# Kernel optimization log

Hardware: AMD Instinct MI355X
Metric: run time of the kernel (lower is better)

Reference implementation:

```python
import jax, jax.numpy as jnp
import numpy as np

EMBED_DIM = 1024
NUM_HEADS = 16
HEAD_DIM = EMBED_DIM // NUM_HEADS
B, S = 2, 2048
BIG = 1e9  # clamp / nan_to_num saturation value from the torch module


def setup_inputs() -> dict:
    key = jax.random.key(0)
    k1, k2, k3, k4, k5 = jax.random.split(key, 5)
    sc = 1.0 / np.sqrt(EMBED_DIM)
    x = jax.random.normal(k1, (B, S, EMBED_DIM), dtype=jnp.float32)
    qkv_w = jax.random.normal(k2, (3 * EMBED_DIM, EMBED_DIM), dtype=jnp.float32) * sc
    qkv_b = jax.random.normal(k3, (3 * EMBED_DIM,), dtype=jnp.float32) * 0.01
    out_w = jax.random.normal(k4, (EMBED_DIM, EMBED_DIM), dtype=jnp.float32) * sc
    out_b = jax.random.normal(k5, (EMBED_DIM,), dtype=jnp.float32) * 0.01
    # causal mask, broadcastable to [B, H, S, S]; 0 => masked
    mask = jnp.tril(jnp.ones((S, S), dtype=jnp.int32))[None, None, :, :]
    return {"x": x, "mask": mask, "qkv_w": qkv_w, "qkv_b": qkv_b,
            "out_w": out_w, "out_b": out_b}


def reference(x, mask, qkv_w, qkv_b, out_w, out_b):
    b, s, e = x.shape
    # fused QKV projection (torch Linear: x @ W.T + b)
    qkv = x @ qkv_w.T + qkv_b                      # [B, S, 3E]
    q, k, v = jnp.split(qkv, 3, axis=-1)
    def heads(t):
        return t.reshape(b, s, NUM_HEADS, HEAD_DIM).transpose(0, 2, 1, 3)  # [B,H,S,D]
    q, k, v = heads(q), heads(k), heads(v)
    scores = jnp.einsum('bhqd,bhkd->bhqk', q, k) / np.sqrt(HEAD_DIM)
    scores = jnp.clip(scores, -BIG, BIG)
    # masked_fill(mask==0, -inf) then nan_to_num(neginf=-1e9) => masked -> -1e9
    scores = jnp.where(mask == 0, -jnp.inf, scores)
    scores = jnp.nan_to_num(scores, nan=0.0, posinf=BIG, neginf=-BIG)
    scores = scores - jnp.max(scores, axis=-1, keepdims=True)
    attn = jax.nn.softmax(scores, axis=-1) + 1e-9
    out = jnp.einsum('bhqk,bhkd->bhqd', attn, v)   # [B,H,S,D]
    out = out.transpose(0, 2, 1, 3).reshape(b, s, e)
    return out @ out_w.T + out_b
```

## Files before the change

### kernel.cpp

```cpp
#include <hip/hip_runtime.h>
#include <stdint.h>

#define B_ 2
#define H_ 16
#define S_ 2048
#define D_ 64
#define E_ 1024
#define M_ 4096
#define N3_ 3072

typedef __attribute__((ext_vector_type(8))) short bf16x8;
typedef __attribute__((ext_vector_type(4))) float f32x4;
typedef __attribute__((ext_vector_type(16))) float f32x16;
typedef __attribute__((ext_vector_type(4))) unsigned short us4;
typedef __attribute__((ext_vector_type(4))) int i32x4;

__device__ __forceinline__ unsigned short f2b(float f) {
  union { float f; unsigned int u; } v; v.f = f;
  unsigned int r = v.u + 0x7FFFu + ((v.u >> 16) & 1u);
  return (unsigned short)(r >> 16);
}

__device__ __forceinline__ void gll16(const void* g, void* l) {
  __builtin_amdgcn_global_load_lds((const __attribute__((address_space(1))) uint32_t*)g,
                                   (__attribute__((address_space(3))) uint32_t*)l, 16, 0, 0);
}

__global__ __launch_bounds__(256) void f32_to_bf16_k(const float* __restrict__ in,
                                                     unsigned short* __restrict__ out, int n) {
  int i = (blockIdx.x * blockDim.x + threadIdx.x) * 4;
  if (i + 3 < n) {
    float4 v = *(const float4*)(in + i);
    us4 o; o.x = f2b(v.x); o.y = f2b(v.y); o.z = f2b(v.z); o.w = f2b(v.w);
    *(us4*)(out + i) = o;
  }
}

template<int MODE>
__global__ __launch_bounds__(512)
void gemm_bt_k(const unsigned short* __restrict__ A,
               const unsigned short* __restrict__ Bw,
               const float* __restrict__ bias,
               float* __restrict__ outf,
               unsigned short* __restrict__ qo,
               unsigned short* __restrict__ ko,
               unsigned short* __restrict__ vto,
               const int K) {
  __shared__ unsigned short As[2][128 * 32];
  __shared__ unsigned short Bs[2][128 * 32];
  const int tid = threadIdx.x;
  const int wid = tid >> 6, lane = tid & 63;
  const int l4 = lane & 15, lh = lane >> 4;
  const int gx = gridDim.x;
  int id = blockIdx.y * gx + blockIdx.x;
  const int cpx = (gx * gridDim.y) >> 3;
  id = (id & 7) * cpx + (id >> 3);
  const int bm = (id / gx) << 7, bn = (id % gx) << 7;
  const int mq = wid >> 2, nq = wid & 3;
  const int wm = mq << 6, wn = nq << 5;
  f32x4 acc[4][2] = {};
  const int srow = lane >> 2;
  const int scolb = ((lane & 3) ^ (((lane >> 3) & 1) << 1)) << 4;
  auto STAGE = [&](int bb, int kt) {
    const int r = (wid << 4) + srow;
    gll16((const char*)A + ((size_t)(bm + r) * K + kt) * 2 + scolb, &As[bb][wid << 9]);
    gll16((const char*)Bw + ((size_t)(bn + r) * K + kt) * 2 + scolb, &Bs[bb][wid << 9]);
  };
  STAGE(0, 0);
  __syncthreads();
  const int ro = (l4 << 5) + ((lh ^ (((l4 >> 1) & 1) << 1)) << 3);
  for (int kt = 0; kt < K; kt += 32) {
    const int bb = (kt >> 5) & 1;
    if (kt + 32 < K) STAGE(bb ^ 1, kt + 32);
    bf16x8 af[4], bfr[2];
#pragma unroll
    for (int g = 0; g < 4; ++g)
      af[g] = *(const bf16x8*)&As[bb][(((mq << 2) + g) << 9) + ro];
#pragma unroll
    for (int h = 0; h < 2; ++h)
      bfr[h] = *(const bf16x8*)&Bs[bb][(((nq << 1) + h) << 9) + ro];
#pragma unroll
    for (int mg = 0; mg < 4; ++mg)
#pragma unroll
      for (int ng = 0; ng < 2; ++ng)
        acc[mg][ng] = __builtin_amdgcn_mfma_f32_16x16x32_bf16(af[mg], bfr[ng], acc[mg][ng], 0, 0, 0);
    __syncthreads();
  }
#pragma unroll
  for (int mg = 0; mg < 4; ++mg) {
#pragma unroll
    for (int ng = 0; ng < 2; ++ng) {
      const int n = bn + wn + (ng << 4) + l4;
      const float bv = bias[n];
      const int m0 = bm + wm + (mg << 4) + (lh << 2);
      if (MODE == 1) {
#pragma unroll
        for (int i = 0; i < 4; ++i)
          outf[(size_t)(m0 + i) * E_ + n] = acc[mg][ng][i] + bv;
      } else {
        const int region = n >> 10;
        const int nn = n & 1023;
        const int h = nn >> 6, d = nn & 63;
        const int b = m0 >> 11, s0 = m0 & 2047;
        const int bh = (b << 4) + h;
        if (region == 2) {
          us4 pk;
#pragma unroll
          for (int i = 0; i < 4; ++i) pk[i] = f2b(acc[mg][ng][i] + bv);
          *(us4*)&vto[((size_t)bh * D_ + d) * S_ + s0] = pk;
        } else {
          unsigned short* dst = (region == 0) ? qo : ko;
          const float sc = (region == 0) ? 0.125f : 1.0f;
#pragma unroll
          for (int i = 0; i < 4; ++i)
            dst[((size_t)bh * S_ + s0 + i) * D_ + d] = f2b((acc[mg][ng][i] + bv) * sc);
        }
      }
    }
  }
}

__global__ __launch_bounds__(256)
void attn_k(const unsigned short* __restrict__ Q,
            const unsigned short* __restrict__ Kt,
            const unsigned short* __restrict__ Vt,
            unsigned short* __restrict__ O) {
  __shared__ __align__(16) char smem[32768];
  const int tid = threadIdx.x;
  const int wid = tid >> 6, lane = tid & 63;
  const int l31 = lane & 31, hi = lane >> 5, hi4 = hi << 2;
  const int bid = blockIdx.x;
  const int xcd = bid & 7, ii = bid >> 3;
  const int bh = (xcd << 2) + (ii & 3);
  const int j = ii >> 2;
  const int qb = (j < 8) ? (15 - j) : (j - 8);
  const int q0w = (qb << 7) + (wid << 5);
  const int nt = (qb + 1) << 1;
  const int ntaw = ((q0w + 31) >> 6) + 1;

  const char* Qb = (const char*)Q + (size_t)bh * (S_ * D_ * 2);
  const char* Kb = (const char*)Kt + (size_t)bh * (S_ * D_ * 2);
  const char* Vb = (const char*)Vt + (size_t)bh * (D_ * S_ * 2);

  bf16x8 qf[4];
#pragma unroll
  for (int st = 0; st < 4; ++st)
    qf[st] = *(const bf16x8*)(Qb + (size_t)(q0w + l31) * 128 + (st << 5) + (hi << 4));

  const int r1 = (wid << 4) + (lane >> 3), r2 = r1 + 8;
  const int cc = lane & 7;
  const int ko1 = (r1 << 7) + ((cc ^ (r1 & 7)) << 4);
  const int ko2 = (r2 << 7) + ((cc ^ (r2 & 7)) << 4);
  const int vo1 = (r1 << 12) + ((cc ^ (r1 & 7)) << 4);
  const int vo2 = (r2 << 12) + ((cc ^ (r2 & 7)) << 4);

  f32x16 oacc[2] = {};
  float m_i = -3.0e38f, l_i = 0.0f;
  const int qg = q0w + l31;
  const int swl = l31 & 7;

  {
    char* kd = smem + (wid << 11);
    char* vd = smem + 16384 + (wid << 11);
    gll16(Kb + ko1, kd); gll16(Kb + ko2, kd + 1024);
    gll16(Vb + vo1, vd); gll16(Vb + vo2, vd + 1024);
  }
  __syncthreads();

  for (int t = 0; t < nt; ++t) {
    const int cur = t & 1;
    if (t + 1 < nt) {
      const int nb = cur ^ 1;
      char* kd = smem + (nb << 13) + (wid << 11);
      char* vd = smem + 16384 + (nb << 13) + (wid << 11);
      gll16(Kb + (size_t)(t + 1) * 8192 + ko1, kd);
      gll16(Kb + (size_t)(t + 1) * 8192 + ko2, kd + 1024);
      gll16(Vb + (size_t)(t + 1) * 128 + vo1, vd);
      gll16(Vb + (size_t)(t + 1) * 128 + vo2, vd + 1024);
    }
    if (t < ntaw) {
      const char* Kc = smem + (cur << 13);
      const char* Vc = smem + 16384 + (cur << 13);
      f32x16 sacc[2] = {};
#pragma unroll
      for (int tt = 0; tt < 2; ++tt)
#pragma unroll
        for (int st = 0; st < 4; ++st) {
          bf16x8 kf = *(const bf16x8*)(Kc + (tt << 12) + (l31 << 7) + ((((st << 1) + hi) ^ swl) << 4));
          sacc[tt] = __builtin_amdgcn_mfma_f32_32x32x16_bf16(kf, qf[st], sacc[tt], 0, 0, 0);
        }
      if (t == ntaw - 1) {
        const int kv0 = t << 6;
#pragma unroll
        for (int tt = 0; tt < 2; ++tt)
#pragma unroll
          for (int r = 0; r < 16; ++r) {
            const int kg = kv0 + (tt << 5) + (r & 3) + ((r >> 2) << 3) + hi4;
            if (kg > qg) sacc[tt][r] = -3.0e38f;
          }
      }
      float pmax = -3.0e38f;
#pragma unroll
      for (int tt = 0; tt < 2; ++tt)
#pragma unroll
        for (int r = 0; r < 16; ++r) pmax = fmaxf(pmax, sacc[tt][r]);
      pmax = fmaxf(pmax, __shfl_xor(pmax, 32));
      if (__any(pmax > m_i + 8.0f)) {
        const float mn = fmaxf(m_i, pmax);
        const float scl = __expf(m_i - mn);
        l_i *= scl;
        m_i = mn;
#pragma unroll
        for (int r = 0; r < 16; ++r) {
          const float sr = __shfl(scl, (r & 3) + ((r >> 2) << 3) + hi4);
          oacc[0][r] *= sr;
          oacc[1][r] *= sr;
        }
      }
#pragma unroll
      for (int tt = 0; tt < 2; ++tt)
#pragma unroll
        for (int r = 0; r < 16; ++r) {
          const float p = __expf(sacc[tt][r] - m_i);
          l_i += p;
          sacc[tt][r] = p;
        }
#pragma unroll
      for (int ks = 0; ks < 4; ++ks) {
        const int tt = ks >> 1, r0 = (ks & 1) << 3;
        int w0, w1, w2, w3;
        asm("v_cvt_pk_bf16_f32 %0, %1, %2" : "=v"(w0) : "v"(sacc[tt][r0 + 0]), "v"(sacc[tt][r0 + 1]));
        asm("v_cvt_pk_bf16_f32 %0, %1, %2" : "=v"(w1) : "v"(sacc[tt][r0 + 2]), "v"(sacc[tt][r0 + 3]));
        asm("v_cvt_pk_bf16_f32 %0, %1, %2" : "=v"(w2) : "v"(sacc[tt][r0 + 4]), "v"(sacc[tt][r0 + 5]));
        asm("v_cvt_pk_bf16_f32 %0, %1, %2" : "=v"(w3) : "v"(sacc[tt][r0 + 6]), "v"(sacc[tt][r0 + 7]));
        asm("v_permlane32_swap_b32 %0, %1" : "+v"(w0), "+v"(w2));
        asm("v_permlane32_swap_b32 %0, %1" : "+v"(w1), "+v"(w3));
        union { i32x4 i; bf16x8 h; } u;
        u.i.x = w0; u.i.y = w1; u.i.z = w2; u.i.w = w3;
        const bf16x8 pa = u.h;
#pragma unroll
        for (int dt = 0; dt < 2; ++dt) {
          bf16x8 vf = *(const bf16x8*)(Vc + (dt << 12) + (l31 << 7) + ((((ks << 1) + hi) ^ swl) << 4));
          oacc[dt] = __builtin_amdgcn_mfma_f32_32x32x16_bf16(pa, vf, oacc[dt], 0, 0, 0);
        }
      }
    }
    __syncthreads();
  }

  const float ltot = l_i + __shfl_xor(l_i, 32);
  const float inv = 1.0f / ltot;
  const int b = bh >> 4, h = bh & 15;
#pragma unroll
  for (int r = 0; r < 16; ++r) {
    const int qr = (r & 3) + ((r >> 2) << 3) + hi4;
    const float ivr = __shfl(inv, qr);
    const size_t off = ((size_t)((b << 11) + q0w + qr) << 10) + (h << 6) + l31;
    O[off]      = f2b(oacc[0][r] * ivr);
    O[off + 32] = f2b(oacc[1][r] * ivr);
  }
}

extern "C" void kernel_launch(void* const* d_in, const int* in_sizes, int n_in,
                              void* d_out, int out_size, void* d_ws, size_t ws_size,
                              hipStream_t stream) {
  const float* x     = (const float*)d_in[0];
  const float* qkv_w = (const float*)d_in[2];
  const float* qkv_b = (const float*)d_in[3];
  const float* out_w = (const float*)d_in[4];
  const float* out_b = (const float*)d_in[5];

  unsigned short* ws   = (unsigned short*)d_ws;
  unsigned short* xb   = ws;
  unsigned short* wqkv = xb + (size_t)M_ * E_;
  unsigned short* wout = wqkv + (size_t)N3_ * E_;
  unsigned short* qB   = wout + (size_t)E_ * E_;
  unsigned short* kB   = qB + (size_t)32 * S_ * D_;
  unsigned short* vtB  = kB + (size_t)32 * S_ * D_;
  unsigned short* oB   = ws;

  f32_to_bf16_k<<<(M_ * E_) / 1024, 256, 0, stream>>>(x, xb, M_ * E_);
  f32_to_bf16_k<<<(N3_ * E_) / 1024, 256, 0, stream>>>(qkv_w, wqkv, N3_ * E_);
  f32_to_bf16_k<<<(E_ * E_) / 1024, 256, 0, stream>>>(out_w, wout, E_ * E_);

  gemm_bt_k<0><<<dim3(N3_ / 128, M_ / 128), 512, 0, stream>>>(
      xb, wqkv, qkv_b, nullptr, qB, kB, vtB, E_);

  attn_k<<<512, 256, 0, stream>>>(qB, kB, vtB, oB);

  gemm_bt_k<1><<<dim3(E_ / 128, M_ / 128), 512, 0, stream>>>(
      oB, wout, out_b, (float*)d_out, nullptr, nullptr, nullptr, E_);
}
```

Baseline: 116.8 us.

## Split attention KV range across two wave groups and fold log2e into Q scale

The attention kernel now runs 512 threads per block: two groups of four waves each handle alternating 64-row halves of a 128-row KV tile for the same query rows. The partial softmax states (max, sum, output) are merged through shared memory at the end. Q is pre-scaled by log2(e)/8 so exp2f can replace __expf, and the rescale threshold is adjusted to match. This doubles per-block parallelism and halves loop iterations, at the cost of doubled LDS, a final cross-group reduction, and the block-order XCD swizzle being removed.

Result: no change. 115.5 us (-1.2%).

```diff
diff --git a/kernel.cpp b/kernel.cpp
--- a/kernel.cpp
+++ b/kernel.cpp
@@ -110,7 +110,7 @@
           *(us4*)&vto[((size_t)bh * D_ + d) * S_ + s0] = pk;
         } else {
           unsigned short* dst = (region == 0) ? qo : ko;
-          const float sc = (region == 0) ? 0.125f : 1.0f;
+          const float sc = (region == 0) ? 0.18033688f : 1.0f;
 #pragma unroll
           for (int i = 0; i < 4; ++i)
             dst[((size_t)bh * S_ + s0 + i) * D_ + d] = f2b((acc[mg][ng][i] + bv) * sc);
@@ -120,23 +120,22 @@
   }
 }
 
-__global__ __launch_bounds__(256)
+__global__ __launch_bounds__(512)
 void attn_k(const unsigned short* __restrict__ Q,
             const unsigned short* __restrict__ Kt,
             const unsigned short* __restrict__ Vt,
             unsigned short* __restrict__ O) {
-  __shared__ __align__(16) char smem[32768];
+  __shared__ __align__(16) char smem[65536];
   const int tid = threadIdx.x;
   const int wid = tid >> 6, lane = tid & 63;
   const int l31 = lane & 31, hi = lane >> 5, hi4 = hi << 2;
+  const int grp = wid >> 2, w4 = wid & 3;
   const int bid = blockIdx.x;
-  const int xcd = bid & 7, ii = bid >> 3;
-  const int bh = (xcd << 2) + (ii & 3);
-  const int j = ii >> 2;
-  const int qb = (j < 8) ? (15 - j) : (j - 8);
-  const int q0w = (qb << 7) + (wid << 5);
-  const int nt = (qb + 1) << 1;
-  const int ntaw = ((q0w + 31) >> 6) + 1;
+  const int bh = bid & 31;
+  const int qb = 15 - (bid >> 5);
+  const int q0w = (qb << 7) + (w4 << 5);
+  const int nt = qb + 1;
+  const int ntaw = (q0w + 31 - (grp << 6) + 128) >> 7;
 
   const char* Qb = (const char*)Q + (size_t)bh * (S_ * D_ * 2);
   const char* Kb = (const char*)Kt + (size_t)bh * (S_ * D_ * 2);
@@ -147,23 +146,26 @@
   for (int st = 0; st < 4; ++st)
     qf[st] = *(const bf16x8*)(Qb + (size_t)(q0w + l31) * 128 + (st << 5) + (hi << 4));
 
-  const int r1 = (wid << 4) + (lane >> 3), r2 = r1 + 8;
   const int cc = lane & 7;
-  const int ko1 = (r1 << 7) + ((cc ^ (r1 & 7)) << 4);
-  const int ko2 = (r2 << 7) + ((cc ^ (r2 & 7)) << 4);
-  const int vo1 = (r1 << 12) + ((cc ^ (r1 & 7)) << 4);
-  const int vo2 = (r2 << 12) + ((cc ^ (r2 & 7)) << 4);
+  const int skr1 = (wid << 4) + (lane >> 3), skr2 = skr1 + 8;
+  const int kgo1 = (skr1 << 7) + ((cc ^ (skr1 & 7)) << 4);
+  const int kgo2 = (skr2 << 7) + ((cc ^ (skr2 & 7)) << 4);
+  const int sd1 = (wid << 3) + (lane >> 4), sd2 = sd1 + 4;
+  const int vhalf = (lane >> 3) & 1;
+  const int vgo1 = (sd1 << 12) + (vhalf << 7) + ((cc ^ (sd1 & 7)) << 4);
+  const int vgo2 = (sd2 << 12) + (vhalf << 7) + ((cc ^ (sd2 & 7)) << 4);
 
   f32x16 oacc[2] = {};
   float m_i = -3.0e38f, l_i = 0.0f;
   const int qg = q0w + l31;
   const int swl = l31 & 7;
+  const int kvg = grp << 6;
 
   {
     char* kd = smem + (wid << 11);
-    char* vd = smem + 16384 + (wid << 11);
-    gll16(Kb + ko1, kd); gll16(Kb + ko2, kd + 1024);
-    gll16(Vb + vo1, vd); gll16(Vb + vo2, vd + 1024);
+    char* vd = smem + 32768 + (wid << 11);
+    gll16(Kb + kgo1, kd); gll16(Kb + kgo2, kd + 1024);
+    gll16(Vb + vgo1, vd); gll16(Vb + vgo2, vd + 1024);
   }
   __syncthreads();
 
@@ -171,26 +173,28 @@
     const int cur = t & 1;
     if (t + 1 < nt) {
       const int nb = cur ^ 1;
-      char* kd = smem + (nb << 13) + (wid << 11);
-      char* vd = smem + 16384 + (nb << 13) + (wid << 11);
-      gll16(Kb + (size_t)(t + 1) * 8192 + ko1, kd);
-      gll16(Kb + (size_t)(t + 1) * 8192 + ko2, kd + 1024);
-      gll16(Vb + (size_t)(t + 1) * 128 + vo1, vd);
-      gll16(Vb + (size_t)(t + 1) * 128 + vo2, vd + 1024);
+      char* kd = smem + (nb << 14) + (wid << 11);
+      char* vd = smem + 32768 + (nb << 14) + (wid << 11);
+      gll16(Kb + (size_t)(t + 1) * 16384 + kgo1, kd);
+      gll16(Kb + (size_t)(t + 1) * 16384 + kgo2, kd + 1024);
+      gll16(Vb + (size_t)(t + 1) * 256 + vgo1, vd);
+      gll16(Vb + (size_t)(t + 1) * 256 + vgo2, vd + 1024);
     }
     if (t < ntaw) {
-      const char* Kc = smem + (cur << 13);
-      const char* Vc = smem + 16384 + (cur << 13);
+      const char* Kc = smem + (cur << 14);
+      const char* Vc = smem + 32768 + (cur << 14);
       f32x16 sacc[2] = {};
 #pragma unroll
-      for (int tt = 0; tt < 2; ++tt)
+      for (int tt = 0; tt < 2; ++tt) {
+        const int kr = kvg + (tt << 5) + l31;
 #pragma unroll
         for (int st = 0; st < 4; ++st) {
-          bf16x8 kf = *(const bf16x8*)(Kc + (tt << 12) + (l31 << 7) + ((((st << 1) + hi) ^ swl) << 4));
+          bf16x8 kf = *(const bf16x8*)(Kc + (kr << 7) + ((((st << 1) + hi) ^ swl) << 4));
           sacc[tt] = __builtin_amdgcn_mfma_f32_32x32x16_bf16(kf, qf[st], sacc[tt], 0, 0, 0);
         }
+      }
       if (t == ntaw - 1) {
-        const int kv0 = t << 6;
+        const int kv0 = (t << 7) + kvg;
 #pragma unroll
         for (int tt = 0; tt < 2; ++tt)
 #pragma unroll
@@ -205,9 +209,9 @@
 #pragma unroll
         for (int r = 0; r < 16; ++r) pmax = fmaxf(pmax, sacc[tt][r]);
       pmax = fmaxf(pmax, __shfl_xor(pmax, 32));
-      if (__any(pmax > m_i + 8.0f)) {
+      if (__any(pmax > m_i + 11.54f)) {
         const float mn = fmaxf(m_i, pmax);
-        const float scl = __expf(m_i - mn);
+        const float scl = exp2f(m_i - mn);
         l_i *= scl;
         m_i = mn;
 #pragma unroll
@@ -221,7 +225,7 @@
       for (int tt = 0; tt < 2; ++tt)
 #pragma unroll
         for (int r = 0; r < 16; ++r) {
-          const float p = __expf(sacc[tt][r] - m_i);
+          const float p = exp2f(sacc[tt][r] - m_i);
           l_i += p;
           sacc[tt][r] = p;
         }
@@ -240,7 +244,8 @@
         const bf16x8 pa = u.h;
 #pragma unroll
         for (int dt = 0; dt < 2; ++dt) {
-          bf16x8 vf = *(const bf16x8*)(Vc + (dt << 12) + (l31 << 7) + ((((ks << 1) + hi) ^ swl) << 4));
+          bf16x8 vf = *(const bf16x8*)(Vc + (((dt << 5) + l31) << 8) + (grp << 7) +
+                                       ((((ks << 1) + hi) ^ swl) << 4));
           oacc[dt] = __builtin_amdgcn_mfma_f32_32x32x16_bf16(pa, vf, oacc[dt], 0, 0, 0);
         }
       }
@@ -248,16 +253,38 @@
     __syncthreads();
   }
 
-  const float ltot = l_i + __shfl_xor(l_i, 32);
-  const float inv = 1.0f / ltot;
-  const int b = bh >> 4, h = bh & 15;
-#pragma unroll
-  for (int r = 0; r < 16; ++r) {
-    const int qr = (r & 3) + ((r >> 2) << 3) + hi4;
-    const float ivr = __shfl(inv, qr);
-    const size_t off = ((size_t)((b << 11) + q0w + qr) << 10) + (h << 6) + l31;
-    O[off]      = f2b(oacc[0][r] * ivr);
-    O[off + 32] = f2b(oacc[1][r] * ivr);
+  l_i += __shfl_xor(l_i, 32);
+
+  float* scrM = (float*)(smem);
+  float* scrL = (float*)(smem + 1024);
+  float* scrO = (float*)(smem + 2048);
+  if (grp == 1) {
+    scrM[(w4 << 6) + lane] = m_i;
+    scrL[(w4 << 6) + lane] = l_i;
+#pragma unroll
+    for (int dt = 0; dt < 2; ++dt)
+#pragma unroll
+      for (int r = 0; r < 16; ++r)
+        scrO[(w4 << 11) + (((dt << 4) + r) << 6) + lane] = oacc[dt][r];
+  }
+  __syncthreads();
+  if (grp == 0) {
+    const float mB = scrM[(w4 << 6) + lane];
+    const float lB = scrL[(w4 << 6) + lane];
+    const float mT = fmaxf(m_i, mB);
+    const float wA = exp2f(m_i - mT), wB = exp2f(mB - mT);
+    const float inv = 1.0f / (l_i * wA + lB * wB);
+    const int b = bh >> 4, h = bh & 15;
+#pragma unroll
+    for (int r = 0; r < 16; ++r) {
+      const int qr = (r & 3) + ((r >> 2) << 3) + hi4;
+      const float wAr = __shfl(wA, qr), wBr = __shfl(wB, qr), ivr = __shfl(inv, qr);
+      const float o0 = scrO[(w4 << 11) + (r << 6) + lane];
+      const float o1 = scrO[(w4 << 11) + ((16 + r) << 6) + lane];
+      const size_t off = ((size_t)((b << 11) + q0w + qr) << 10) + (h << 6) + l31;
+      O[off]      = f2b((oacc[0][r] * wAr + o0 * wBr) * ivr);
+      O[off + 32] = f2b((oacc[1][r] * wAr + o1 * wBr) * ivr);
+    }
   }
 }
 
@@ -286,7 +313,7 @@
   gemm_bt_k<0><<<dim3(N3_ / 128, M_ / 128), 512, 0, stream>>>(
       xb, wqkv, qkv_b, nullptr, qB, kB, vtB, E_);
 
-  attn_k<<<512, 256, 0, stream>>>(qB, kB, vtB, oB);
+  attn_k<<<512, 512, 0, stream>>>(qB, kB, vtB, oB);
 
   gemm_bt_k<1><<<dim3(E_ / 128, M_ / 128), 512, 0, stream>>>(
       oB, wout, out_b, (float*)d_out, nullptr, nullptr, nullptr, E_);
```
